# Performance work log

Measured on AMD Instinct MI355X. Metric: run time of the kernel, lower is better.

## Reference

```python
import jax, jax.numpy as jnp
import numpy as np

RADIUS = 3.4
NSAMPLE = 5


def setup_inputs() -> dict:
    key = jax.random.key(0)
    x = jax.random.normal(key, (8, 4096, 3), dtype=jnp.float32)
    return {"x": x}


def reference(x) -> jnp.ndarray:
    # pointnet2 ball_query(radius=3.4, nsample=5, xyz=x, new_xyz=x)
    # For each query point, take the first NSAMPLE point indices (in scan order)
    # with squared distance < radius^2; if fewer than NSAMPLE found, remaining
    # slots hold the FIRST found index (CUDA kernel fills row with first hit).
    r2 = jnp.float32(RADIUS * RADIUS)
    sq = jnp.sum(x * x, axis=-1)  # [B, N]
    # d2[b, q, k] = ||x_q - x_k||^2
    d2 = sq[:, :, None] + sq[:, None, :] - 2.0 * jnp.einsum("bqd,bkd->bqk", x, x)
    mask = d2 < r2  # [B, Nq, N]
    # 0-based rank of each True entry along the scan axis
    cum = jnp.cumsum(mask.astype(jnp.int32), axis=-1)
    rank = cum - mask.astype(jnp.int32)  # rank among hits, valid where mask
    first_idx = jnp.argmax(mask, axis=-1).astype(jnp.int32)  # [B, Nq] (0 if none)
    slots = []
    for j in range(NSAMPLE):
        sel = mask & (rank == j)
        has_j = jnp.any(sel, axis=-1)
        idx_j = jnp.argmax(sel, axis=-1).astype(jnp.int32)
        slots.append(jnp.where(has_j, idx_j, first_idx))
    return jnp.stack(slots, axis=-1)  # [B, Nq, NSAMPLE] int32
```

## Files before the change

### kernel.cpp

```cpp
#include <hip/hip_runtime.h>


#pragma clang fp contract(off)

#define BQ_N 4096
#define BQ_B 8
#define BQ_NS 5

__global__ __launch_bounds__(1024) void ball_query_kernel(
    const float* __restrict__ x, int* __restrict__ out, float r2) {
  const int wid = (blockIdx.x * 1024 + threadIdx.x) >> 6;
  const int lane = threadIdx.x & 63;
  const int group = lane >> 4;
  const int sub = lane & 15;

  const int qidx = wid * 4 + group;
  const int b = qidx >> 12;
  const int q = qidx & (BQ_N - 1);

  const float* xb = x + (size_t)b * BQ_N * 3;

  const float qx = xb[q * 3 + 0];
  const float qy = xb[q * 3 + 1];
  const float qz = xb[q * 3 + 2];
  const float kx0 = xb[sub * 3 + 0];
  const float ky0 = xb[sub * 3 + 1];
  const float kz0 = xb[sub * 3 + 2];

  const float sq_q = (qx * qx + qy * qy) + qz * qz;
  const float sqk0 = (kx0 * kx0 + ky0 * ky0) + kz0 * kz0;
  const float dot0 = (qx * kx0 + qy * ky0) + qz * kz0;
  const float d20 = (sq_q + sqk0) - 2.0f * dot0;

  const int base = qidx * BQ_NS;
  const unsigned sublow = (1u << sub) - 1u;

  const unsigned long long m1 = __ballot(d20 < r2);
  const unsigned mg1 = (unsigned)(m1 >> (group * 16)) & 0xFFFFu;
  if (d20 < r2) {
    const int rank = __popc(mg1 & sublow);
    if (rank < BQ_NS) out[base + rank] = sub;
  }
  int cnt = __popc(mg1);

  if (__any(cnt < BQ_NS)) {
    int first = (mg1 != 0u) ? (__ffs(mg1) - 1) : -1;
    for (int k0 = 16; k0 < BQ_N && __any(cnt < BQ_NS); k0 += 16) {
      const int k = k0 + sub;
      const float kx = xb[k * 3 + 0];
      const float ky = xb[k * 3 + 1];
      const float kz = xb[k * 3 + 2];
      const float sqk = (kx * kx + ky * ky) + kz * kz;
      const float dot = (qx * kx + qy * ky) + qz * kz;
      const float d2 = (sq_q + sqk) - 2.0f * dot;
      const bool h = (d2 < r2) && (cnt < BQ_NS + 16);
      const unsigned long long m = __ballot(d2 < r2);
      const unsigned mg = (unsigned)(m >> (group * 16)) & 0xFFFFu;
      if (h && cnt < BQ_NS) {
        const int rank = cnt + __popc(mg & sublow);
        if (rank < BQ_NS) out[base + rank] = k;
      }
      if (first < 0 && mg != 0u) first = k0 + __ffs(mg) - 1;
      if (cnt < BQ_NS) cnt += __popc(mg);
    }
    if (sub == 0 && cnt < BQ_NS) {
      for (int j = (cnt < 1 ? 1 : cnt); j < BQ_NS; ++j) out[base + j] = first;
    }
  }
}

extern "C" void kernel_launch(void* const* d_in, const int* in_sizes, int n_in,
                              void* d_out, int out_size, void* d_ws, size_t ws_size,
                              hipStream_t stream) {
  const float* x = (const float*)d_in[0];
  int* out = (int*)d_out;
  const float r2 = 3.4f * 3.4f;

  const int total_waves = (BQ_B * BQ_N) / 4;
  const int block = 1024;
  const int grid = total_waves / 16;
  ball_query_kernel<<<grid, block, 0, stream>>>(x, out, r2);
}
```

Measured before the change: 54.40 us.

## Process unfinished queries serially with full-wave 128-point scan chunks

The fallback scan no longer splits the wave into four 16-lane groups that each scan 16 points per step. It now loops over the four queries and skips any that are already satisfied. Each remaining query is scanned by the whole 64-lane wave, 128 points per iteration in two ballots. This removes the waste of finished groups idling while one group keeps scanning. The cost is that unfinished queries are handled one after another, and each step adds shuffles and clamped loads.

```diff
diff --git a/kernel.cpp b/kernel.cpp
--- a/kernel.cpp
+++ b/kernel.cpp
@@ -44,27 +44,63 @@
   int cnt = __popc(mg1);
 
   if (__any(cnt < BQ_NS)) {
-    int first = (mg1 != 0u) ? (__ffs(mg1) - 1) : -1;
-    for (int k0 = 16; k0 < BQ_N && __any(cnt < BQ_NS); k0 += 16) {
-      const int k = k0 + sub;
-      const float kx = xb[k * 3 + 0];
-      const float ky = xb[k * 3 + 1];
-      const float kz = xb[k * 3 + 2];
-      const float sqk = (kx * kx + ky * ky) + kz * kz;
-      const float dot = (qx * kx + qy * ky) + qz * kz;
-      const float d2 = (sq_q + sqk) - 2.0f * dot;
-      const bool h = (d2 < r2) && (cnt < BQ_NS + 16);
-      const unsigned long long m = __ballot(d2 < r2);
-      const unsigned mg = (unsigned)(m >> (group * 16)) & 0xFFFFu;
-      if (h && cnt < BQ_NS) {
-        const int rank = cnt + __popc(mg & sublow);
-        if (rank < BQ_NS) out[base + rank] = k;
+    const int first0 = (mg1 != 0u) ? (__ffs(mg1) - 1) : -1;
+    const unsigned long long lanelow = (1ull << lane) - 1ull;
+
+    for (int g = 0; g < 4; ++g) {
+      int cntg = __shfl(cnt, g * 16);
+      if (cntg >= BQ_NS) continue;
+      int firstg = __shfl(first0, g * 16);
+      const float gqx = __shfl(qx, g * 16);
+      const float gqy = __shfl(qy, g * 16);
+      const float gqz = __shfl(qz, g * 16);
+      const float gsq = __shfl(sq_q, g * 16);
+      const int gbase = (wid * 4 + g) * BQ_NS;
+
+      for (int k0 = 16; k0 < BQ_N && cntg < BQ_NS; k0 += 128) {
+        const int ka = k0 + lane;
+        const int kb = ka + 64;
+        const int kca = (ka < BQ_N) ? ka : (BQ_N - 1);
+        const int kcb = (kb < BQ_N) ? kb : (BQ_N - 1);
+        const float ax = xb[kca * 3 + 0];
+        const float ay = xb[kca * 3 + 1];
+        const float az = xb[kca * 3 + 2];
+        const float bx = xb[kcb * 3 + 0];
+        const float by = xb[kcb * 3 + 1];
+        const float bz = xb[kcb * 3 + 2];
+
+        const float sqa = (ax * ax + ay * ay) + az * az;
+        const float dota = (gqx * ax + gqy * ay) + gqz * az;
+        const float d2a = (gsq + sqa) - 2.0f * dota;
+        const float sqb = (bx * bx + by * by) + bz * bz;
+        const float dotb = (gqx * bx + gqy * by) + gqz * bz;
+        const float d2b = (gsq + sqb) - 2.0f * dotb;
+
+        const bool ha = (d2a < r2) && (ka < BQ_N);
+        const bool hb = (d2b < r2) && (kb < BQ_N);
+        const unsigned long long ma = __ballot(ha);
+        const unsigned long long mb = __ballot(hb);
+
+        if (ha && cntg < BQ_NS) {
+          const int rank = cntg + __popcll(ma & lanelow);
+          if (rank < BQ_NS) out[gbase + rank] = ka;
+        }
+        const int cnta = cntg + __popcll(ma);
+        if (hb && cnta < BQ_NS) {
+          const int rank = cnta + __popcll(mb & lanelow);
+          if (rank < BQ_NS) out[gbase + rank] = kb;
+        }
+        if (firstg < 0) {
+          if (ma)      firstg = k0 + __builtin_ctzll(ma);
+          else if (mb) firstg = k0 + 64 + __builtin_ctzll(mb);
+        }
+        cntg = cnta + __popcll(mb);
       }
-      if (first < 0 && mg != 0u) first = k0 + __ffs(mg) - 1;
-      if (cnt < BQ_NS) cnt += __popc(mg);
-    }
-    if (sub == 0 && cnt < BQ_NS) {
-      for (int j = (cnt < 1 ? 1 : cnt); j < BQ_NS; ++j) out[base + j] = first;
+
+      if (lane == 0 && cntg < BQ_NS) {
+        const int s = (cntg < 1) ? 1 : cntg;
+        for (int j = s; j < BQ_NS; ++j) out[gbase + j] = firstg;
+      }
     }
   }
 }
```

Result: no change. 53.56 us (-1.6%).
